# Optimization experiments

Measured on AMD Instinct MI355X. Metric: run time of the kernel, lower is better.

## Reference

```python
import jax, jax.numpy as jnp
import numpy as np

N_NODES = 100000
N_EDGES = 3200000
IN_DIM = 64


def gcn_conv(x, edge_index, edge_weight, W, b, num_nodes):
    """PyG GCNConv: h = x @ W; add self-loops (w=1); symmetric norm; scatter-add; + bias."""
    src = edge_index[0]
    dst = edge_index[1]
    loop = jnp.arange(num_nodes)
    src_a = jnp.concatenate([src, loop])
    dst_a = jnp.concatenate([dst, loop])
    w_a = jnp.concatenate([edge_weight, jnp.ones((num_nodes,), dtype=edge_weight.dtype)])
    # degree at target nodes (weighted, incl. self-loops)
    deg = jax.ops.segment_sum(w_a, dst_a, num_segments=num_nodes)
    dinv = jnp.where(deg > 0, jax.lax.rsqrt(deg), 0.0)
    norm = dinv[src_a] * w_a * dinv[dst_a]  # [E+N]
    h = x @ W  # [N, out] - transform before propagate (cheaper: out_dim small)
    msg = h[src_a] * norm[:, None]  # [E+N, out]
    out = jax.ops.segment_sum(msg, dst_a, num_segments=num_nodes)
    return out + b


def setup_inputs() -> dict:
    key = jax.random.key(0)
    ks = jax.random.split(key, 9)
    x = jax.random.normal(ks[0], (N_NODES, IN_DIM), dtype=jnp.float32)
    edge_index = jax.random.randint(ks[1], (2, N_EDGES), 0, N_NODES, dtype=jnp.int64)
    edge_weight = jax.random.uniform(ks[2], (N_EDGES,), dtype=jnp.float32)
    s1 = 1.0 / np.sqrt(IN_DIM)
    W1 = jax.random.uniform(ks[3], (IN_DIM, 16), jnp.float32, -s1, s1)
    b1 = jnp.zeros((16,), jnp.float32)
    s2 = 1.0 / np.sqrt(16)
    W2 = jax.random.uniform(ks[4], (16, 2), jnp.float32, -s2, s2)
    b2 = jnp.zeros((2,), jnp.float32)
    s3 = 1.0 / np.sqrt(2)
    lin_w = jax.random.uniform(ks[5], (2, 1), jnp.float32, -s3, s3)
    lin_b = jax.random.uniform(ks[6], (1,), jnp.float32, -s3, s3)
    return {"x": x, "edge_index": edge_index, "edge_weight": edge_weight,
            "W1": W1, "b1": b1, "W2": W2, "b2": b2, "lin_w": lin_w, "lin_b": lin_b}


def reference(x, edge_index, edge_weight, W1, b1, W2, b2, lin_w, lin_b):
    h = gcn_conv(x, edge_index, edge_weight, W1, b1, N_NODES)
    h = jax.nn.relu(h)
    # F.dropout in eval mode = identity (deterministic reference)
    x2 = gcn_conv(h, edge_index, edge_weight, W2, b2, N_NODES)  # [N, 2]
    out = jax.nn.relu(x2)
    out = jax.nn.sigmoid(out @ lin_w + lin_b)  # [N, 1]
    return (out, x2)
```

## Files before the change

kernel.cpp:

```cpp
#include <hip/hip_runtime.h>
#include <math.h>

#define N_NODES 100000
#define N_EDGES 3200000
#define LO_BITS 7
#define NPB 128
#define NB  ((N_NODES + NPB - 1) / NPB)
#define PART_B 512
#define PART_T 1024
#define CPB (N_EDGES / PART_B)
#define BCAP 5120
#define CMAX 10

typedef unsigned long long u64;
typedef unsigned int u32;
typedef unsigned short u16;

static __device__ inline u16 f2bf(float f) {
    u32 u = __float_as_uint(f);
    return (u16)((u + 0x7FFF + ((u >> 16) & 1)) >> 16);
}
static __device__ inline float bf2f(u16 h) {
    return __uint_as_float((u32)h << 16);
}

static __device__ inline int wave_iscan(int x, int lane) {
#pragma unroll
    for (int off = 1; off < 64; off <<= 1) {
        int u = __shfl_up(x, off, 64);
        if (lane >= off) x += u;
    }
    return x;
}


__global__ void __launch_bounds__(PART_T) hist_k(const int* __restrict__ dst,
                                                 int* __restrict__ hist_mat) {
    __shared__ int h[NB];
    for (int t = threadIdx.x; t < NB; t += blockDim.x) h[t] = 0;
    __syncthreads();
    int base = blockIdx.x * CPB;
    for (int it = 0; it < (CPB + PART_T - 1) / PART_T; it++) {
        int e = base + it * PART_T + threadIdx.x;
        if (e < base + CPB) {
            int d = dst[e];
            atomicAdd(&h[d >> LO_BITS], 1);
        }
    }
    __syncthreads();
    for (int t = threadIdx.x; t < NB; t += blockDim.x)
        hist_mat[blockIdx.x * NB + t] = h[t];
}

__global__ void __launch_bounds__(PART_B) colscan_k(const int* __restrict__ hist_mat,
                                                    int* __restrict__ hist_excl,
                                                    int* __restrict__ tot) {
    __shared__ int wsum[PART_B / 64];
    int bin = blockIdx.x, t = threadIdx.x;
    int lane = t & 63, w = t >> 6;
    int v = hist_mat[t * NB + bin];
    int x = wave_iscan(v, lane);
    if (lane == 63) wsum[w] = x;
    __syncthreads();
    int base = 0;
#pragma unroll
    for (int i = 0; i < PART_B / 64; i++)
        if (i < w) base += wsum[i];
    hist_excl[t * NB + bin] = base + x - v;
    if (t == PART_B - 1) tot[bin] = base + x;
}

__global__ void base_k(const int* __restrict__ tot, int* __restrict__ bbase) {
    __shared__ int wsum[16];
    int t = threadIdx.x, lane = t & 63, w = t >> 6;
    int v = (t < NB) ? tot[t] : 0;
    int x = wave_iscan(v, lane);
    if (lane == 63) wsum[w] = x;
    __syncthreads();
    int base = 0;
#pragma unroll
    for (int i = 0; i < 16; i++)
        if (i < w) base += wsum[i];
    if (t < NB) bbase[t] = base + x - v;
    if (t == 0) bbase[NB] = N_EDGES;
}

__global__ void __launch_bounds__(PART_T) part_k(
        const int* __restrict__ src, const int* __restrict__ dst,
        const float* __restrict__ w, const int* __restrict__ hist_mat,
        const int* __restrict__ hist_excl,
        const int* __restrict__ bbase, u64* __restrict__ ebuf) {
    __shared__ u64 sorted[CPB];
    __shared__ int cur[NB];
    __shared__ int gofs[NB];
    __shared__ int swsum[PART_T / 64];
    int t = threadIdx.x;
    int lane = t & 63, wv = t >> 6;
    int base = blockIdx.x * CPB;
    int rawc = (t < NB) ? hist_mat[blockIdx.x * NB + t] : 0;
    int x = wave_iscan(rawc, lane);
    if (lane == 63) swsum[wv] = x;
    __syncthreads();
    int bs = 0;
#pragma unroll
    for (int i = 0; i < PART_T / 64; i++)
        if (i < wv) bs += swsum[i];
    if (t < NB) {
        int lscan = bs + x - rawc;
        cur[t] = lscan;
        gofs[t] = bbase[t] + hist_excl[blockIdx.x * NB + t] - lscan;
    }
    __syncthreads();
#pragma unroll
    for (int it = 0; it < (CPB + PART_T - 1) / PART_T; it++) {
        int e = base + it * PART_T + t;
        if (e < base + CPB) {
            int d = dst[e];
            int sv = __builtin_nontemporal_load(&src[e]);
            u32 wvv = __float_as_uint(__builtin_nontemporal_load(&w[e]));
            int pos = atomicAdd(&cur[d >> LO_BITS], 1);
            sorted[pos] = ((u64)(u32)sv << 47) | ((u64)(u32)d << 30) | (u64)(wvv >> 2);
        }
    }
    __syncthreads();
    for (int p = t; p < CPB; p += PART_T) {
        u64 pk = sorted[p];
        int sv = (int)(pk >> 47);
        int d  = (int)((pk >> 30) & 0x1FFFF);
        u32 wvv = ((u32)pk & 0x3FFFFFFF) << 2;
        u32 hi = ((u32)sv << LO_BITS) | (u32)(d & (NPB - 1));
        ebuf[gofs[d >> LO_BITS] + p] = ((u64)hi << 32) | (u64)wvv;
    }
}

__global__ void __launch_bounds__(512) csr_deg_k(
        const u64* __restrict__ ebuf, const int* __restrict__ bbase,
        int* __restrict__ row_ptr, float* __restrict__ dinv,
        u64* __restrict__ pedge) {
    __shared__ u64 staged[BCAP];
    __shared__ int   cnt[NPB];
    __shared__ float wsum[NPB];
    __shared__ int   cur[NPB];
    __shared__ int   cw[2];
    int b = blockIdx.x, t = threadIdx.x;
    if (t < NPB) { cnt[t] = 0; wsum[t] = 0.0f; }
    __syncthreads();
    int j0 = bbase[b], j1 = bbase[b + 1];
    u64 pe[CMAX];
    int nit = 0;
#pragma unroll
    for (int it = 0; it < CMAX; it++) {
        int j = j0 + it * 512 + t;
        if (j < j1) {
            u64 e = ebuf[j];
            pe[it] = e;
            int lo = (int)((u32)(e >> 32) & (NPB - 1));
            atomicAdd(&cnt[lo], 1);
            atomicAdd(&wsum[lo], __uint_as_float((u32)e));
            nit = it + 1;
        }
    }
    for (int j = j0 + 512 * CMAX + t; j < j1; j += 512) {
        u64 e = ebuf[j];
        int lo = (int)((u32)(e >> 32) & (NPB - 1));
        atomicAdd(&cnt[lo], 1);
        atomicAdd(&wsum[lo], __uint_as_float((u32)e));
    }
    __syncthreads();
    int lane = t & 63;
    int v = (t < NPB) ? cnt[t] : 0;
    int x = wave_iscan(v, lane);
    if (t < NPB && lane == 63) cw[t >> 6] = x;
    __syncthreads();
    if (t < NPB) {
        int incl = x + ((t >= 64) ? cw[0] : 0);
        int excl = incl - v;
        cur[t] = excl;
        int node = b * NPB + t;
        if (node < N_NODES) {
            row_ptr[node] = j0 + excl;
            dinv[node] = rsqrtf(1.0f + wsum[t]);
        }
    }
    if (b == NB - 1 && t == 0) row_ptr[N_NODES] = N_EDGES;
    __syncthreads();
#pragma unroll
    for (int it = 0; it < CMAX; it++) {
        if (it < nit) {
            u64 e = pe[it];
            u32 hi = (u32)(e >> 32);
            int lo = (int)(hi & (NPB - 1));
            int p = atomicAdd(&cur[lo], 1);
            u64 val = ((u64)(hi >> LO_BITS) << 32) | (u64)(u32)e;
            if (p < BCAP) staged[p] = val;
            else pedge[j0 + p] = val;
        }
    }
    for (int j = j0 + 512 * CMAX + t; j < j1; j += 512) {
        u64 e = ebuf[j];
        u32 hi = (u32)(e >> 32);
        int lo = (int)(hi & (NPB - 1));
        int p = atomicAdd(&cur[lo], 1);
        u64 val = ((u64)(hi >> LO_BITS) << 32) | (u64)(u32)e;
        if (p < BCAP) staged[p] = val;
        else pedge[j0 + p] = val;
    }
    __syncthreads();
    int nbe = j1 - j0;
    int lim = nbe < BCAP ? nbe : BCAP;
    for (int p = t; p < lim; p += 512) pedge[j0 + p] = staged[p];
}


__global__ void __launch_bounds__(256) gemm1(
        const float* __restrict__ x, const float* __restrict__ W1,
        const float* __restrict__ dinv, u16* __restrict__ g1b) {
    __shared__ float sW[64 * 16];
    __shared__ float xs[16][68];
    for (int t = threadIdx.x; t < 64 * 16; t += blockDim.x) sW[t] = W1[t];
    int nbase = blockIdx.x * 16;
    {
        int q = threadIdx.x;
        const float4 v = ((const float4*)(x + (size_t)nbase * 64))[q];
        int n = q >> 4, f4 = q & 15;
        xs[n][f4 * 4 + 0] = v.x;
        xs[n][f4 * 4 + 1] = v.y;
        xs[n][f4 * 4 + 2] = v.z;
        xs[n][f4 * 4 + 3] = v.w;
    }
    __syncthreads();
    int n = threadIdx.x >> 4, c = threadIdx.x & 15;
    int node = nbase + n;
    float acc = 0.0f;
#pragma unroll
    for (int k = 0; k < 64; k++) acc += xs[n][k] * sW[k * 16 + c];
    g1b[node * 16 + c] = f2bf(acc * dinv[node]);
}

__global__ void gather1(const int* __restrict__ row_ptr, const u64* __restrict__ pedge,
                        const float* __restrict__ dinv, const u32* __restrict__ g1w,
                        const float* __restrict__ b1, const float* __restrict__ W2,
                        float* __restrict__ y2) {
    int gid = blockIdx.x * blockDim.x + threadIdx.x;
    int node = gid >> 6;
    if (node >= N_NODES) return;
    int lane = threadIdx.x & 63;
    int c2 = lane & 7;
    int eg = lane >> 3;
    int j0 = row_ptr[node], j1 = row_ptr[node + 1];
    float a0 = 0.0f, a1 = 0.0f;
    for (int base = j0; base < j1; base += 64) {
        int idx = base + lane;
        u64 se = (idx < j1) ? __builtin_nontemporal_load(&pedge[idx]) : 0ULL;
#pragma unroll
        for (int k = 0; k < 8; k++) {
            u64 pe = __shfl(se, k * 8 + eg, 64);
            int s = (int)(pe >> 32);
            float wr = __uint_as_float((u32)pe);
            u32 g2 = g1w[s * 8 + c2];
            a0 += bf2f((u16)g2) * wr;
            a1 += bf2f((u16)(g2 >> 16)) * wr;
        }
    }
    a0 += __shfl_xor(a0, 8, 64);  a1 += __shfl_xor(a1, 8, 64);
    a0 += __shfl_xor(a0, 16, 64); a1 += __shfl_xor(a1, 16, 64);
    a0 += __shfl_xor(a0, 32, 64); a1 += __shfl_xor(a1, 32, 64);
    u32 gs = g1w[node * 8 + c2];
    a0 += bf2f((u16)gs);
    a1 += bf2f((u16)(gs >> 16));
    float di = dinv[node];
    int c0 = c2 * 2, c1 = c0 + 1;
    float v0 = a0 * di + b1[c0]; v0 = v0 > 0.0f ? v0 : 0.0f;
    float v1 = a1 * di + b1[c1]; v1 = v1 > 0.0f ? v1 : 0.0f;
    float p0 = v0 * W2[c0 * 2]     + v1 * W2[c1 * 2];
    float p1 = v0 * W2[c0 * 2 + 1] + v1 * W2[c1 * 2 + 1];
    p0 += __shfl_xor(p0, 1, 64); p1 += __shfl_xor(p1, 1, 64);
    p0 += __shfl_xor(p0, 2, 64); p1 += __shfl_xor(p1, 2, 64);
    p0 += __shfl_xor(p0, 4, 64); p1 += __shfl_xor(p1, 4, 64);
    if (lane == 0) {
        y2[node * 2]     = p0 * di;
        y2[node * 2 + 1] = p1 * di;
    }
}

__global__ void gather2(const int* __restrict__ row_ptr, const u64* __restrict__ pedge,
                        const float* __restrict__ dinv, const float* __restrict__ y2,
                        const float* __restrict__ b2, const float* __restrict__ lin_w,
                        const float* __restrict__ lin_b, float* __restrict__ out) {
    int gid = blockIdx.x * blockDim.x + threadIdx.x;
    int i = gid >> 6;
    if (i >= N_NODES) return;
    int lane = threadIdx.x & 63;
    int k = lane & 1;
    int el = lane >> 1;
    int j0 = row_ptr[i], j1 = row_ptr[i + 1];
    float a = 0.0f;
    for (int base = j0; base < j1; base += 64) {
        int idx = base + lane;
        u64 se = (idx < j1) ? __builtin_nontemporal_load(&pedge[idx]) : 0ULL;
#pragma unroll
        for (int k2 = 0; k2 < 2; k2++) {
            u64 pe = __shfl(se, k2 * 32 + el, 64);
            int s = (int)(pe >> 32);
            float wr = __uint_as_float((u32)pe);
            a += y2[s * 2 + k] * wr;
        }
    }
    a += __shfl_xor(a, 2, 64);
    a += __shfl_xor(a, 4, 64);
    a += __shfl_xor(a, 8, 64);
    a += __shfl_xor(a, 16, 64);
    a += __shfl_xor(a, 32, 64);
    float ao = __shfl_xor(a, 1, 64);
    if (lane == 0) {
        float di = dinv[i];
        float y0 = y2[i * 2], y1 = y2[i * 2 + 1];
        float x20 = (a + y0) * di + b2[0];
        float x21 = (ao + y1) * di + b2[1];
        out[N_NODES + i * 2]     = x20;
        out[N_NODES + i * 2 + 1] = x21;
        float r0 = x20 > 0.0f ? x20 : 0.0f;
        float r1 = x21 > 0.0f ? x21 : 0.0f;
        float z = r0 * lin_w[0] + r1 * lin_w[1] + lin_b[0];
        out[i] = 1.0f / (1.0f + expf(-z));
    }
}

extern "C" void kernel_launch(void* const* d_in, const int* in_sizes, int n_in,
                              void* d_out, int out_size, void* d_ws, size_t ws_size,
                              hipStream_t stream) {
    const float* x     = (const float*)d_in[0];
    const int*   ei    = (const int*)d_in[1];
    const float* ew    = (const float*)d_in[2];
    const float* W1    = (const float*)d_in[3];
    const float* b1    = (const float*)d_in[4];
    const float* W2    = (const float*)d_in[5];
    const float* b2    = (const float*)d_in[6];
    const float* lin_w = (const float*)d_in[7];
    const float* lin_b = (const float*)d_in[8];
    float* out = (float*)d_out;

    const int* src = ei;
    const int* dst = ei + N_EDGES;

    char* w8 = (char*)d_ws;
    size_t off = 0;
    auto take = [&](size_t bytes) { char* p = w8 + off; off += (bytes + 15) & ~((size_t)15); return (void*)p; };
    u64*   ebuf      = (u64*)  take((size_t)N_EDGES * 8);
    u64*   pedge     = (u64*)  take((size_t)N_EDGES * 8);
    int*   hist_mat  = (int*)  take((size_t)PART_B * NB * 4);
    int*   hist_excl = (int*)  take((size_t)PART_B * NB * 4);
    int*   tot       = (int*)  take((size_t)NB * 4);
    int*   bbase     = (int*)  take((size_t)(NB + 1) * 4);
    int*   row_ptr   = (int*)  take((size_t)(N_NODES + 1) * 4);
    float* dinv      = (float*)take((size_t)N_NODES * 4);
    u16*   g1b       = (u16*)ebuf;
    u32*   g1w       = (u32*)ebuf;
    float* y2        = (float*)ebuf + (size_t)8 * N_NODES;

    const int B = 256;

    hist_k<<<PART_B, PART_T, 0, stream>>>(dst, hist_mat);
    colscan_k<<<NB, PART_B, 0, stream>>>(hist_mat, hist_excl, tot);
    base_k<<<1, 1024, 0, stream>>>(tot, bbase);
    part_k<<<PART_B, PART_T, 0, stream>>>(src, dst, ew, hist_mat, hist_excl, bbase, ebuf);

    csr_deg_k<<<NB, 512, 0, stream>>>(ebuf, bbase, row_ptr, dinv, pedge);

    gemm1<<<N_NODES / 16, B, 0, stream>>>(x, W1, dinv, g1b);
    gather1<<<(64 * N_NODES + B - 1) / B, B, 0, stream>>>(row_ptr, pedge, dinv, g1w, b1, W2, y2);

    gather2<<<(64 * N_NODES + B - 1) / B, B, 0, stream>>>(row_ptr, pedge, dinv, y2, b2,
                                                         lin_w, lin_b, out);
}
```

Measured before the change: 247.5 us.

## Gather full feature rows per edge lane and reduce with transpose-shuffle butterflies

In both gather kernels each lane now owns one edge and loads the whole source row: two 16-byte vector loads of the 16 bf16 features in layer one, one float2 in layer two. Previously the edges were broadcast by shuffle and each lane fetched only one 32-bit or 32-bit-float slice. Accumulation runs in 16 registers per lane and is combined with a recursive-halving shuffle butterfly, so each lane ends up holding one feature's total. This cuts the number of shuffles and memory instructions per edge but raises register pressure, and it only uses all 64 lanes when a node has at least 64 edges.

```diff
diff --git a/kernel.cpp b/kernel.cpp
--- a/kernel.cpp
+++ b/kernel.cpp
@@ -245,38 +245,71 @@
     int node = gid >> 6;
     if (node >= N_NODES) return;
     int lane = threadIdx.x & 63;
-    int c2 = lane & 7;
-    int eg = lane >> 3;
     int j0 = row_ptr[node], j1 = row_ptr[node + 1];
-    float a0 = 0.0f, a1 = 0.0f;
+    float a[16];
+#pragma unroll
+    for (int f = 0; f < 16; f++) a[f] = 0.0f;
     for (int base = j0; base < j1; base += 64) {
         int idx = base + lane;
-        u64 se = (idx < j1) ? __builtin_nontemporal_load(&pedge[idx]) : 0ULL;
-#pragma unroll
-        for (int k = 0; k < 8; k++) {
-            u64 pe = __shfl(se, k * 8 + eg, 64);
-            int s = (int)(pe >> 32);
-            float wr = __uint_as_float((u32)pe);
-            u32 g2 = g1w[s * 8 + c2];
-            a0 += bf2f((u16)g2) * wr;
-            a1 += bf2f((u16)(g2 >> 16)) * wr;
-        }
-    }
-    a0 += __shfl_xor(a0, 8, 64);  a1 += __shfl_xor(a1, 8, 64);
-    a0 += __shfl_xor(a0, 16, 64); a1 += __shfl_xor(a1, 16, 64);
-    a0 += __shfl_xor(a0, 32, 64); a1 += __shfl_xor(a1, 32, 64);
-    u32 gs = g1w[node * 8 + c2];
-    a0 += bf2f((u16)gs);
-    a1 += bf2f((u16)(gs >> 16));
+        u64 pe = (idx < j1) ? __builtin_nontemporal_load(&pedge[idx]) : 0ULL;
+        int s = (int)(pe >> 32);
+        float wr = __uint_as_float((u32)pe);
+        const uint4* rp = (const uint4*)(g1w + (size_t)s * 8);
+        uint4 r0 = rp[0];
+        uint4 r1 = rp[1];
+        u32 rw0 = r0.x, rw1 = r0.y, rw2 = r0.z, rw3 = r0.w;
+        u32 rw4 = r1.x, rw5 = r1.y, rw6 = r1.z, rw7 = r1.w;
+        a[0]  += bf2f((u16)rw0) * wr;  a[1]  += bf2f((u16)(rw0 >> 16)) * wr;
+        a[2]  += bf2f((u16)rw1) * wr;  a[3]  += bf2f((u16)(rw1 >> 16)) * wr;
+        a[4]  += bf2f((u16)rw2) * wr;  a[5]  += bf2f((u16)(rw2 >> 16)) * wr;
+        a[6]  += bf2f((u16)rw3) * wr;  a[7]  += bf2f((u16)(rw3 >> 16)) * wr;
+        a[8]  += bf2f((u16)rw4) * wr;  a[9]  += bf2f((u16)(rw4 >> 16)) * wr;
+        a[10] += bf2f((u16)rw5) * wr;  a[11] += bf2f((u16)(rw5 >> 16)) * wr;
+        a[12] += bf2f((u16)rw6) * wr;  a[13] += bf2f((u16)(rw6 >> 16)) * wr;
+        a[14] += bf2f((u16)rw7) * wr;  a[15] += bf2f((u16)(rw7 >> 16)) * wr;
+    }
+    bool h0 = (lane & 1) != 0;
+    float t8[8];
+#pragma unroll
+    for (int f = 0; f < 8; f++) {
+        float send = h0 ? a[f] : a[f + 8];
+        float keep = h0 ? a[f + 8] : a[f];
+        t8[f] = keep + __shfl_xor(send, 1, 64);
+    }
+    bool h1 = (lane & 2) != 0;
+    float t4[4];
+#pragma unroll
+    for (int f = 0; f < 4; f++) {
+        float send = h1 ? t8[f] : t8[f + 4];
+        float keep = h1 ? t8[f + 4] : t8[f];
+        t4[f] = keep + __shfl_xor(send, 2, 64);
+    }
+    bool h2 = (lane & 4) != 0;
+    float t2[2];
+#pragma unroll
+    for (int f = 0; f < 2; f++) {
+        float send = h2 ? t4[f] : t4[f + 2];
+        float keep = h2 ? t4[f + 2] : t4[f];
+        t2[f] = keep + __shfl_xor(send, 4, 64);
+    }
+    bool h3 = (lane & 8) != 0;
+    float send = h3 ? t2[0] : t2[1];
+    float keep = h3 ? t2[1] : t2[0];
+    float tot = keep + __shfl_xor(send, 8, 64);
+    tot += __shfl_xor(tot, 16, 64);
+    tot += __shfl_xor(tot, 32, 64);
+    int f = (h0 ? 8 : 0) + (h1 ? 4 : 0) + (h2 ? 2 : 0) + (h3 ? 1 : 0);
+    u32 gs = g1w[node * 8 + (f >> 1)];
+    float self = bf2f((u16)((f & 1) ? (gs >> 16) : (gs & 0xFFFF)));
     float di = dinv[node];
-    int c0 = c2 * 2, c1 = c0 + 1;
-    float v0 = a0 * di + b1[c0]; v0 = v0 > 0.0f ? v0 : 0.0f;
-    float v1 = a1 * di + b1[c1]; v1 = v1 > 0.0f ? v1 : 0.0f;
-    float p0 = v0 * W2[c0 * 2]     + v1 * W2[c1 * 2];
-    float p1 = v0 * W2[c0 * 2 + 1] + v1 * W2[c1 * 2 + 1];
+    float vf = (tot + self) * di + b1[f];
+    vf = vf > 0.0f ? vf : 0.0f;
+    float p0 = vf * W2[2 * f];
+    float p1 = vf * W2[2 * f + 1];
     p0 += __shfl_xor(p0, 1, 64); p1 += __shfl_xor(p1, 1, 64);
     p0 += __shfl_xor(p0, 2, 64); p1 += __shfl_xor(p1, 2, 64);
     p0 += __shfl_xor(p0, 4, 64); p1 += __shfl_xor(p1, 4, 64);
+    p0 += __shfl_xor(p0, 8, 64); p1 += __shfl_xor(p1, 8, 64);
     if (lane == 0) {
         y2[node * 2]     = p0 * di;
         y2[node * 2 + 1] = p1 * di;
@@ -291,21 +324,21 @@
     int i = gid >> 6;
     if (i >= N_NODES) return;
     int lane = threadIdx.x & 63;
-    int k = lane & 1;
-    int el = lane >> 1;
     int j0 = row_ptr[i], j1 = row_ptr[i + 1];
-    float a = 0.0f;
+    float a0 = 0.0f, a1 = 0.0f;
     for (int base = j0; base < j1; base += 64) {
         int idx = base + lane;
-        u64 se = (idx < j1) ? __builtin_nontemporal_load(&pedge[idx]) : 0ULL;
-#pragma unroll
-        for (int k2 = 0; k2 < 2; k2++) {
-            u64 pe = __shfl(se, k2 * 32 + el, 64);
-            int s = (int)(pe >> 32);
-            float wr = __uint_as_float((u32)pe);
-            a += y2[s * 2 + k] * wr;
-        }
-    }
+        u64 pe = (idx < j1) ? __builtin_nontemporal_load(&pedge[idx]) : 0ULL;
+        int s = (int)(pe >> 32);
+        float wr = __uint_as_float((u32)pe);
+        float2 yv = *(const float2*)(y2 + (size_t)s * 2);
+        a0 += yv.x * wr;
+        a1 += yv.y * wr;
+    }
+    bool h0 = (lane & 1) != 0;
+    float send = h0 ? a0 : a1;
+    float keep = h0 ? a1 : a0;
+    float a = keep + __shfl_xor(send, 1, 64);
     a += __shfl_xor(a, 2, 64);
     a += __shfl_xor(a, 4, 64);
     a += __shfl_xor(a, 8, 64);
```

After: 248.8 us. No clear change (+0.5%).
